# Optimization experiments

Measured on AMD Instinct MI355X. Metric: run time of the kernel, lower is better.

Reference implementation:

```python
import jax, jax.numpy as jnp
import numpy as np

# Problem dims (match init_kwargs)
M, P, TINI, NH, TT, NB = 4, 6, 50, 100, 2000, 4096
L = TT - TINI - NH + 1  # 1851, dimension of g
NC = TINI * M + TINI * P + P  # 506 equality constraints
DELTA = 1e-6  # tiny ridge on g so the KKT system is nonsingular (u,y unchanged to ~1e-6)


def block_hankel(w, Lr, d):
    """w: flat [T*d] time series (d-dim samples stacked). Returns [Lr*d, T-Lr+1].
    H[d*i+k, j] = w[d*(i+j)+k] = w[row + d*j]."""
    T = w.shape[0] // d
    cols = T - Lr + 1
    return w[jnp.arange(Lr * d)[:, None] + d * jnp.arange(cols)[None, :]]


def setup_inputs() -> dict:
    key = jax.random.key(0)
    ks = jax.random.split(key, 7)
    ud = jax.random.normal(ks[0], (TT, M), jnp.float32)          # input data series
    yd = jax.random.normal(ks[1], (TT, P), jnp.float32)          # output data series
    q = 10.0 + 0.1 * jax.random.normal(ks[2], (P * NH,), jnp.float32)  # diag of Q (positive)
    r = 10.0 + 0.1 * jax.random.normal(ks[3], (M * NH,), jnp.float32)  # diag of R (positive)
    ref = jax.random.normal(ks[4], (NB, NH * P), jnp.float32)
    u_ini = jax.random.normal(ks[5], (NB, TINI * M), jnp.float32)
    y_ini = jax.random.normal(ks[6], (NB, TINI * P), jnp.float32)
    return {"ud": ud, "yd": yd, "q": q, "r": r, "ref": ref, "u_ini": u_ini, "y_ini": y_ini}


def reference(ud, yd, q, r, ref, u_ini, y_ini):
    # Block-Hankel data matrices (the module's U, Y Parameters)
    U = block_hankel(ud.reshape(-1), TINI + NH, M)  # [(Tini+N)*m, L]
    Y = block_hankel(yd.reshape(-1), TINI + NH, P)  # [(Tini+N)*p, L]
    Up, Uf = U[: M * TINI], U[M * TINI:]            # [Tini*m, L], [N*m, L]
    Yp, Yf = Y[: P * TINI], Y[P * TINI:]            # [Tini*p, L], [N*p, L]

    # Deterministic (linear, non-stochastic) DeePC QP with inactive box constraints:
    #   min_g (Yf g - ref)^T Q (Yf g - ref) + (Uf g)^T R (Uf g)
    #   s.t.  Up g = u_ini, Yp g = y_ini, (Yf g)[-p:] = ref[-p:]
    # Solved exactly via the KKT system (unique in u = Uf g, y = Yf g).
    H = Yf.T @ (q[:, None] * Yf) + Uf.T @ (r[:, None] * Uf) + DELTA * jnp.eye(L, dtype=ud.dtype)
    A = jnp.concatenate([Up, Yp, Yf[-P:]], axis=0)  # [NC, L]
    KKT = jnp.block([
        [2.0 * H, A.T],
        [A, jnp.zeros((NC, NC), dtype=ud.dtype)],
    ])  # [L+NC, L+NC]

    rhs = jnp.concatenate([
        2.0 * (Yf.T @ (q[:, None] * ref.T)),  # [L, NB] gradient term
        u_ini.T,                               # [Tini*m, NB]
        y_ini.T,                               # [Tini*p, NB]
        ref[:, -P:].T,                          # [p, NB] terminal constraint
    ], axis=0)

    g = jnp.linalg.solve(KKT, rhs)[:L]  # [L, NB]
    inp = Uf @ g   # optimal input  [N*m, NB]
    out = Yf @ g   # optimal output [N*p, NB]
    return inp, out
```

## Files before the change

kernel.cpp:

```cpp
#include <hip/hip_runtime.h>
#include <hip/hip_bf16.h>

#define LDIM   1851
#define NFR    1000
#define NAR    506
#define NCRP   1536
#define LDC    1856
#define NG     1024
#define NS     512
#define NXC    1152
#define LDMA   1120
#define NBATCH 4096
#define NOUT   1000
#define INVDP  500000.0

#define OFF_C     ((size_t)0)
#define SZ_C      ((size_t)NCRP * LDC * 4)
#define OFF_ILG   OFF_C
#define OFF_ILS   (OFF_C + 8388608)
#define OFF_GCC   (OFF_C + SZ_C)
#define SZ_GCC    ((size_t)NCRP * NCRP * 8)
#define OFF_G     (OFF_GCC + SZ_GCC)
#define SZ_G      ((size_t)NG * NG * 8)
#define OFF_TA    (OFF_G + SZ_G)
#define SZ_TA     ((size_t)NG * NS * 8)
#define OFF_S     (OFF_TA + SZ_TA)
#define SZ_S      ((size_t)NS * NS * 8)
#define OFF_X12   (OFF_S + SZ_S)
#define SZ_X12    ((size_t)NS * NXC * 8)
#define OFF_MRAW  (OFF_X12 + SZ_X12)
#define SZ_MRAW   ((size_t)NG * NXC * 4)
#define OFF_XB    OFF_MRAW
#define OFF_MALL  (OFF_MRAW + SZ_MRAW)
#define SZ_MALL   ((size_t)NG * LDMA * 4)
#define OFF_IDG   OFF_MALL
#define OFF_IDS   (OFF_MALL + 524288)
#define OFF_INALL (OFF_MALL + SZ_MALL)
#define SZ_INALL  ((size_t)LDMA * NBATCH * 4)
#define OFF_TB    OFF_INALL
#define OFF_TINV  (OFF_INALL + 4194304)

__device__ __forceinline__ double dweight(int i, const float* q, const float* r) {
  return (i < 400) ? (double)r[i] : (double)q[i - 400];
}

__global__ __launch_bounds__(256) void k_build_C(const float* __restrict__ ud,
                                                 const float* __restrict__ yd,
                                                 float* __restrict__ C) {
  int j = blockIdx.x * 256 + threadIdx.x;
  int rr = blockIdx.y;
  if (j >= LDC) return;
  float v = 0.f;
  if (j < LDIM) {
    if (rr < 400)        v = ud[200 + rr + 4 * j];
    else if (rr < 1000)  v = yd[300 + (rr - 400) + 6 * j];
    else if (rr < 1200)  v = ud[(rr - 1000) + 4 * j];
    else if (rr < 1500)  v = yd[(rr - 1200) + 6 * j];
    else if (rr < 1506)  v = yd[894 + (rr - 1500) + 6 * j];
  }
  C[(size_t)rr * LDC + j] = v;
}

__global__ __launch_bounds__(256) void k_gram(const float* __restrict__ C,
                                              double* __restrict__ GCC) {
  int ti = blockIdx.y, tj = blockIdx.x;
  if (ti < tj) return;
  __shared__ float As[64][33];
  __shared__ float Bs[64][33];
  int tid = threadIdx.x;
  int tr4 = (tid >> 4) * 4, tc4 = (tid & 15) * 4;
  double acc[4][4] = {};
  int i0 = ti * 64, j0 = tj * 64;
  for (int k0 = 0; k0 < LDC; k0 += 32) {
#pragma unroll
    for (int l = 0; l < 8; ++l) {
      int t = tid + l * 256;
      int rr = t >> 5, cc = t & 31;
      As[rr][cc] = C[(size_t)(i0 + rr) * LDC + k0 + cc];
      Bs[rr][cc] = C[(size_t)(j0 + rr) * LDC + k0 + cc];
    }
    __syncthreads();
#pragma unroll
    for (int kk = 0; kk < 32; ++kk) {
      double a[4], b[4];
#pragma unroll
      for (int i = 0; i < 4; ++i) a[i] = (double)As[tr4 + i][kk];
#pragma unroll
      for (int jx = 0; jx < 4; ++jx) b[jx] = (double)Bs[tc4 + jx][kk];
#pragma unroll
      for (int i = 0; i < 4; ++i)
#pragma unroll
        for (int jx = 0; jx < 4; ++jx) acc[i][jx] += a[i] * b[jx];
    }
    __syncthreads();
  }
#pragma unroll
  for (int i = 0; i < 4; ++i)
#pragma unroll
    for (int jx = 0; jx < 4; ++jx) {
      int gi = i0 + tr4 + i, gj = j0 + tc4 + jx;
      GCC[(size_t)gi * NCRP + gj] = acc[i][jx];
      if (ti != tj) GCC[(size_t)gj * NCRP + gi] = acc[i][jx];
    }
}

__global__ __launch_bounds__(256) void k_copyG(const double* __restrict__ GCC,
                                               const float* __restrict__ q,
                                               const float* __restrict__ r,
                                               double* __restrict__ G) {
  int idx = blockIdx.x * 256 + threadIdx.x;
  int i = idx >> 10, j = idx & 1023;
  double v = (i < NFR && j < NFR) ? GCC[(size_t)i * NCRP + j] : 0.0;
  if (i == j) {
    if (i < NFR) v += 1e-6 / dweight(i, q, r);
    else v = 1.0;
  }
  G[idx] = v;
}

__global__ __launch_bounds__(256) void k_copyTA(const double* __restrict__ GCC,
                                                double* __restrict__ TA) {
  int idx = blockIdx.x * 256 + threadIdx.x;
  int f = idx >> 9, a = idx & 511;
  TA[idx] = (f < NFR && a < NAR) ? GCC[(size_t)f * NCRP + 1000 + a] : 0.0;
}

__global__ __launch_bounds__(256) void k_potrf_inv(double* __restrict__ M, int ld, int k,
                                                   double* __restrict__ IDG) {
  __shared__ double T[64][65];
  __shared__ double invd[64];
  int tid = threadIdx.x;
#pragma unroll
  for (int l = 0; l < 16; ++l) {
    int t = tid + l * 256;
    T[t >> 6][t & 63] = M[(size_t)(k + (t >> 6)) * ld + k + (t & 63)];
  }
  __syncthreads();
  for (int c = 0; c < 64; ++c) {
    if (tid == 0) T[c][c] = sqrt(T[c][c]);
    __syncthreads();
    double piv = T[c][c];
    for (int rr = c + 1 + tid; rr < 64; rr += 256) T[rr][c] /= piv;
    __syncthreads();
    for (int t = tid; t < 64 * 64; t += 256) {
      int rr = t >> 6, jj = t & 63;
      if (rr > c && jj > c) T[rr][jj] -= T[rr][c] * T[jj][c];
    }
    __syncthreads();
  }
#pragma unroll
  for (int l = 0; l < 16; ++l) {
    int t = tid + l * 256;
    M[(size_t)(k + (t >> 6)) * ld + k + (t & 63)] = T[t >> 6][t & 63];
  }
  __syncthreads();
  if (tid < 64) invd[tid] = 1.0 / T[tid][tid];
  __syncthreads();
  if (tid < 64) {
    int c = tid;
    for (int r = c + 1; r < 64; ++r) {
      double s = T[r][c] * invd[c];
      for (int j = c + 1; j < r; ++j) s += T[r][j] * T[c][j];
      T[c][r] = -s * invd[r];
    }
  }
  __syncthreads();
#pragma unroll
  for (int l = 0; l < 16; ++l) {
    int t = tid + l * 256;
    int r = t >> 6, c = t & 63;
    IDG[t] = (r < c) ? 0.0 : (r == c ? invd[r] : T[c][r]);
  }
}

__global__ __launch_bounds__(256) void k_trsm_inv(double* __restrict__ M, int ld, int k,
                                                  const double* __restrict__ IDG) {
  __shared__ double As[64][33];
  __shared__ double Bs[32][65];
  int tid = threadIdx.x;
  int tr4 = (tid >> 4) * 4, tc4 = (tid & 15) * 4;
  int r0 = k + 64 + blockIdx.x * 64;
  double acc[4][4] = {};
  for (int k0 = 0; k0 < 64; k0 += 32) {
#pragma unroll
    for (int l = 0; l < 8; ++l) {
      int t = tid + l * 256;
      As[t >> 5][t & 31] = M[(size_t)(r0 + (t >> 5)) * ld + k + k0 + (t & 31)];
    }
#pragma unroll
    for (int l = 0; l < 8; ++l) {
      int t = tid + l * 256;
      int kk = t >> 6, cc = t & 63;
      Bs[kk][cc] = IDG[cc * 64 + k0 + kk];
    }
    __syncthreads();
#pragma unroll
    for (int kk = 0; kk < 32; ++kk) {
      double a[4], b[4];
#pragma unroll
      for (int i = 0; i < 4; ++i) a[i] = As[tr4 + i][kk];
#pragma unroll
      for (int jx = 0; jx < 4; ++jx) b[jx] = Bs[kk][tc4 + jx];
#pragma unroll
      for (int i = 0; i < 4; ++i)
#pragma unroll
        for (int jx = 0; jx < 4; ++jx) acc[i][jx] += a[i] * b[jx];
    }
    __syncthreads();
  }
#pragma unroll
  for (int i = 0; i < 4; ++i)
#pragma unroll
    for (int jx = 0; jx < 4; ++jx)
      M[(size_t)(r0 + tr4 + i) * ld + k + tc4 + jx] = acc[i][jx];
}

__global__ __launch_bounds__(256) void k_chol_syrk(double* __restrict__ M, int ld, int k) {
  int ti = blockIdx.y, tj = blockIdx.x;
  if (ti < tj) return;
  __shared__ double Pa[64][33];
  __shared__ double Pb[64][33];
  int tid = threadIdx.x;
  int tr4 = (tid >> 4) * 4, tc4 = (tid & 15) * 4;
  int i0 = k + 64 + ti * 64, j0 = k + 64 + tj * 64;
  double acc[4][4] = {};
  for (int k0 = 0; k0 < 64; k0 += 32) {
#pragma unroll
    for (int l = 0; l < 8; ++l) {
      int t = tid + l * 256;
      int rr = t >> 5, cc = t & 31;
      Pa[rr][cc] = M[(size_t)(i0 + rr) * ld + k + k0 + cc];
      Pb[rr][cc] = M[(size_t)(j0 + rr) * ld + k + k0 + cc];
    }
    __syncthreads();
#pragma unroll
    for (int kk = 0; kk < 32; ++kk) {
      double a[4], b[4];
#pragma unroll
      for (int i = 0; i < 4; ++i) a[i] = Pa[tr4 + i][kk];
#pragma unroll
      for (int jx = 0; jx < 4; ++jx) b[jx] = Pb[tc4 + jx][kk];
#pragma unroll
      for (int i = 0; i < 4; ++i)
#pragma unroll
        for (int jx = 0; jx < 4; ++jx) acc[i][jx] += a[i] * b[jx];
    }
    __syncthreads();
  }
#pragma unroll
  for (int i = 0; i < 4; ++i)
#pragma unroll
    for (int jx = 0; jx < 4; ++jx)
      M[(size_t)(i0 + tr4 + i) * ld + j0 + tc4 + jx] -= acc[i][jx];
}

__device__ __forceinline__ void dgemm_nn_core(const double* __restrict__ A, int lda,
                                              const double* __restrict__ B, int ldb,
                                              double* __restrict__ C, int ldc,
                                              int kBeg, int kEnd, double alpha) {
  __shared__ double As[64][33];
  __shared__ double Bs[32][65];
  int tid = threadIdx.x;
  int tr4 = (tid >> 4) * 4, tc4 = (tid & 15) * 4;
  double acc[4][4] = {};
  for (int k0 = kBeg; k0 < kEnd; k0 += 32) {
#pragma unroll
    for (int l = 0; l < 8; ++l) {
      int t = tid + l * 256;
      As[t >> 5][t & 31] = A[(size_t)(t >> 5) * lda + k0 + (t & 31)];
    }
#pragma unroll
    for (int l = 0; l < 8; ++l) {
      int t = tid + l * 256;
      Bs[t >> 6][t & 63] = B[(size_t)(k0 + (t >> 6)) * ldb + (t & 63)];
    }
    __syncthreads();
#pragma unroll
    for (int kk = 0; kk < 32; ++kk) {
      double a[4], b[4];
#pragma unroll
      for (int i = 0; i < 4; ++i) a[i] = As[tr4 + i][kk];
#pragma unroll
      for (int jx = 0; jx < 4; ++jx) b[jx] = Bs[kk][tc4 + jx];
#pragma unroll
      for (int i = 0; i < 4; ++i)
#pragma unroll
        for (int jx = 0; jx < 4; ++jx) acc[i][jx] += a[i] * b[jx];
    }
    __syncthreads();
  }
#pragma unroll
  for (int i = 0; i < 4; ++i)
#pragma unroll
    for (int jx = 0; jx < 4; ++jx)
      C[(size_t)(tr4 + i) * ldc + tc4 + jx] = alpha * acc[i][jx];
}

__device__ __forceinline__ void dgemm_tn_core(const double* __restrict__ A, int lda,
                                              const double* __restrict__ B, int ldb,
                                              double* __restrict__ C, int ldc,
                                              int kBeg, int kEnd, double alpha) {
  __shared__ double Ls[32][65];
  __shared__ double Bs[32][65];
  int tid = threadIdx.x;
  int tr4 = (tid >> 4) * 4, tc4 = (tid & 15) * 4;
  double acc[4][4] = {};
  for (int k0 = kBeg; k0 < kEnd; k0 += 32) {
#pragma unroll
    for (int l = 0; l < 8; ++l) {
      int t = tid + l * 256;
      int jj = t >> 6, rr = t & 63;
      Ls[jj][rr] = A[(size_t)(k0 + jj) * lda + rr];
    }
#pragma unroll
    for (int l = 0; l < 8; ++l) {
      int t = tid + l * 256;
      Bs[t >> 6][t & 63] = B[(size_t)(k0 + (t >> 6)) * ldb + (t & 63)];
    }
    __syncthreads();
#pragma unroll
    for (int kk = 0; kk < 32; ++kk) {
      double a[4], b[4];
#pragma unroll
      for (int i = 0; i < 4; ++i) a[i] = Ls[kk][tr4 + i];
#pragma unroll
      for (int jx = 0; jx < 4; ++jx) b[jx] = Bs[kk][tc4 + jx];
#pragma unroll
      for (int i = 0; i < 4; ++i)
#pragma unroll
        for (int jx = 0; jx < 4; ++jx) acc[i][jx] += a[i] * b[jx];
    }
    __syncthreads();
  }
#pragma unroll
  for (int i = 0; i < 4; ++i)
#pragma unroll
    for (int jx = 0; jx < 4; ++jx)
      C[(size_t)(tr4 + i) * ldc + tc4 + jx] = alpha * acc[i][jx];
}

__global__ __launch_bounds__(256) void k_dgemm_nn(const double* __restrict__ A, int lda,
                                                  const double* __restrict__ B, int ldb,
                                                  double* __restrict__ C, int ldc,
                                                  int K, int tri, double alpha) {
  int bi = blockIdx.y, bj = blockIdx.x;
  int kEnd = tri ? ((bi + 1) * 64 < K ? (bi + 1) * 64 : K) : K;
  dgemm_nn_core(A + (size_t)bi * 64 * lda, lda, B + bj * 64, ldb,
                C + (size_t)bi * 64 * ldc + bj * 64, ldc, 0, kEnd, alpha);
}

__global__ __launch_bounds__(256) void k_dgemm_tn(const double* __restrict__ A, int lda,
                                                  const double* __restrict__ B, int ldb,
                                                  double* __restrict__ C, int ldc,
                                                  int K, int tri, double alpha) {
  int bi = blockIdx.y, bj = blockIdx.x;
  int kBeg = tri ? bi * 64 : 0;
  dgemm_tn_core(A + bi * 64, lda, B + bj * 64, ldb,
                C + (size_t)bi * 64 * ldc + bj * 64, ldc, kBeg, K, alpha);
}

__global__ __launch_bounds__(256) void k_init_iL(double* __restrict__ iL, int nShift,
                                                 const double* __restrict__ IDIAG) {
  int idx = blockIdx.x * 256 + threadIdx.x;
  int n = 1 << nShift;
  int i = idx >> nShift, j = idx & (n - 1);
  int d = i >> 6;
  double v = 0.0;
  if ((j >> 6) == d) v = IDIAG[(size_t)d * 4096 + (i & 63) * 64 + (j & 63)];
  iL[idx] = v;
}

__global__ __launch_bounds__(256) void k_ilv_tmp(const double* __restrict__ L, int ldl,
                                                 const double* __restrict__ iL, int ldi,
                                                 double* __restrict__ T, int half) {
  int p = blockIdx.z, bi = blockIdx.y, bj = blockIdx.x;
  int base = p * 2 * half;
  dgemm_nn_core(L + (size_t)(base + half + bi * 64) * ldl + base, ldl,
                iL + (size_t)base * ldi + base + bj * 64, ldi,
                T + (size_t)p * half * half + (size_t)bi * 64 * half + bj * 64, half,
                0, half, 1.0);
}

__global__ __launch_bounds__(256) void k_ilv_fin(double* __restrict__ iL, int ldi,
                                                 const double* __restrict__ T, int half) {
  int p = blockIdx.z, bi = blockIdx.y, bj = blockIdx.x;
  int base = p * 2 * half;
  dgemm_nn_core(iL + (size_t)(base + half + bi * 64) * ldi + base + half, ldi,
                T + (size_t)p * half * half + bj * 64, half,
                iL + (size_t)(base + half + bi * 64) * ldi + base + bj * 64, ldi,
                0, half, -1.0);
}

__global__ __launch_bounds__(256) void k_buildS(const double* __restrict__ GCC,
                                                const double* __restrict__ TA,
                                                double* __restrict__ S) {
  __shared__ double Ga[64][33];
  __shared__ double Tb[32][65];
  int tid = threadIdx.x;
  int tr4 = (tid >> 4) * 4, tc4 = (tid & 15) * 4;
  int a0 = blockIdx.y * 64, b0 = blockIdx.x * 64;
  double acc[4][4] = {};
  for (int f0 = 0; f0 < NG; f0 += 32) {
#pragma unroll
    for (int l = 0; l < 8; ++l) {
      int t = tid + l * 256;
      int rr = t >> 5, cc = t & 31;
      Ga[rr][cc] = GCC[(size_t)(1000 + a0 + rr) * NCRP + f0 + cc];
    }
#pragma unroll
    for (int l = 0; l < 8; ++l) {
      int t = tid + l * 256;
      int rr = t >> 6, cc = t & 63;
      Tb[rr][cc] = TA[(size_t)(f0 + rr) * NS + b0 + cc];
    }
    __syncthreads();
#pragma unroll
    for (int kk = 0; kk < 32; ++kk) {
      double a[4], b[4];
#pragma unroll
      for (int i = 0; i < 4; ++i) a[i] = Ga[tr4 + i][kk];
#pragma unroll
      for (int jx = 0; jx < 4; ++jx) b[jx] = Tb[kk][tc4 + jx];
#pragma unroll
      for (int i = 0; i < 4; ++i)
#pragma unroll
        for (int jx = 0; jx < 4; ++jx) acc[i][jx] += a[i] * b[jx];
    }
    __syncthreads();
  }
#pragma unroll
  for (int i = 0; i < 4; ++i)
#pragma unroll
    for (int jx = 0; jx < 4; ++jx) {
      int a = a0 + tr4 + i, b = b0 + tc4 + jx;
      double v;
      if (a < NAR && b < NAR)
        v = (GCC[(size_t)(1000 + a) * NCRP + 1000 + b] - acc[i][jx]) * INVDP;
      else
        v = (a == b) ? 1.0 : 0.0;
      S[(size_t)a * NS + b] = v;
    }
}

__global__ __launch_bounds__(256) void k_build_x12rhs(const double* __restrict__ TA,
                                                      double* __restrict__ X12) {
  int c = blockIdx.x * 256 + threadIdx.x;
  int a = blockIdx.y;
  if (c >= NXC) return;
  double v = 0.0;
  if (a < NAR) {
    if (c < 600) v = TA[(size_t)(400 + c) * NS + a];
    else if (c < 1106) v = (a == (c - 600)) ? 1.0 : 0.0;
  }
  X12[(size_t)a * NXC + c] = v;
}

__global__ __launch_bounds__(256) void k_gemm_M(const double* __restrict__ TA,
                                                const double* __restrict__ X12,
                                                const float* __restrict__ q,
                                                const float* __restrict__ r,
                                                float* __restrict__ Mraw) {
  __shared__ double Ga[64][33];
  __shared__ double Xb[32][65];
  int tid = threadIdx.x;
  int tr4 = (tid >> 4) * 4, tc4 = (tid & 15) * 4;
  int o0 = blockIdx.y * 64, c0 = blockIdx.x * 64;
  double acc[4][4] = {};
  for (int k0 = 0; k0 < NS; k0 += 32) {
#pragma unroll
    for (int l = 0; l < 8; ++l) {
      int t = tid + l * 256;
      int rr = t >> 5, cc = t & 31;
      Ga[rr][cc] = TA[(size_t)(o0 + rr) * NS + k0 + cc];
    }
#pragma unroll
    for (int l = 0; l < 8; ++l) {
      int t = tid + l * 256;
      int rr = t >> 6, cc = t & 63;
      Xb[rr][cc] = X12[(size_t)(k0 + rr) * NXC + c0 + cc];
    }
    __syncthreads();
#pragma unroll
    for (int kk = 0; kk < 32; ++kk) {
      double a[4], b[4];
#pragma unroll
      for (int i = 0; i < 4; ++i) a[i] = Ga[tr4 + i][kk];
#pragma unroll
      for (int jx = 0; jx < 4; ++jx) b[jx] = Xb[kk][tc4 + jx];
#pragma unroll
      for (int i = 0; i < 4; ++i)
#pragma unroll
        for (int jx = 0; jx < 4; ++jx) acc[i][jx] += a[i] * b[jx];
    }
    __syncthreads();
  }
#pragma unroll
  for (int i = 0; i < 4; ++i)
#pragma unroll
    for (int jx = 0; jx < 4; ++jx) {
      int o = o0 + tr4 + i, col = c0 + tc4 + jx;
      float v = 0.f;
      if (o < NFR) {
        double scale = 1.0 / (2.0 * dweight(o, q, r));
        double t = acc[i][jx] * scale;
        v = (float)((col < 600) ? -t : t);
      }
      Mraw[(size_t)o * NXC + col] = v;
    }
}

__global__ __launch_bounds__(256) void k_assemble_M(const float* __restrict__ Mraw,
                                                    float* __restrict__ Mall) {
  int j = blockIdx.x * 256 + threadIdx.x;
  int o = blockIdx.y;
  if (j >= LDMA) return;
  float v = 0.f;
  if (j < 600) {
    v = Mraw[(size_t)o * NXC + j];
    if (o == 400 + j) v += 1.0f;
    if (j >= 594) v += Mraw[(size_t)o * NXC + 1100 + (j - 594)];
  } else if (j < 1100) {
    v = Mraw[(size_t)o * NXC + j];
  }
  Mall[(size_t)o * LDMA + j] = v;
}

__global__ __launch_bounds__(256) void k_transpose_in(const float* __restrict__ ref,
                                                      const float* __restrict__ ui,
                                                      const float* __restrict__ yi,
                                                      float* __restrict__ INall) {
  __shared__ float t[32][33];
  int tx = threadIdx.x & 31, ty = threadIdx.x >> 5;
  int n0 = blockIdx.x * 32, j0 = blockIdx.y * 32;
#pragma unroll
  for (int p = 0; p < 4; ++p) {
    int nb = n0 + ty + p * 8;
    int j = j0 + tx;
    float v = 0.f;
    if (j < 600)        v = ref[(size_t)nb * 600 + j];
    else if (j < 800)   v = ui[(size_t)nb * 200 + (j - 600)];
    else if (j < 1100)  v = yi[(size_t)nb * 300 + (j - 800)];
    t[ty + p * 8][tx] = v;
  }
  __syncthreads();
#pragma unroll
  for (int p = 0; p < 4; ++p) {
    INall[(size_t)(j0 + ty + p * 8) * NBATCH + n0 + tx] = t[tx][ty + p * 8];
  }
}

__global__ __launch_bounds__(256) void k_gemm_out(const float* __restrict__ Mall,
                                                  const float* __restrict__ INall,
                                                  float* __restrict__ out) {
  __shared__ float As[32][132];
  __shared__ float Bs[32][132];
  int tid = threadIdx.x;
  int tr = tid >> 4, tc = tid & 15;
  int m0 = blockIdx.y * 128, n0 = blockIdx.x * 128;
  float acc[8][8] = {};
  for (int k0 = 0; k0 < LDMA; k0 += 32) {
#pragma unroll
    for (int l = 0; l < 16; ++l) {
      int t = tid + l * 256;
      int rr = t >> 5, cc = t & 31;
      As[cc][rr] = Mall[(size_t)(m0 + rr) * LDMA + k0 + cc];
    }
#pragma unroll
    for (int l = 0; l < 16; ++l) {
      int t = tid + l * 256;
      int rr = t >> 7, cc = t & 127;
      Bs[rr][cc] = INall[(size_t)(k0 + rr) * NBATCH + n0 + cc];
    }
    __syncthreads();
#pragma unroll
    for (int kk = 0; kk < 32; ++kk) {
      float4 a0 = *(const float4*)&As[kk][tr * 4];
      float4 a1 = *(const float4*)&As[kk][64 + tr * 4];
      float4 b0 = *(const float4*)&Bs[kk][tc * 4];
      float4 b1 = *(const float4*)&Bs[kk][64 + tc * 4];
      float av[8] = {a0.x, a0.y, a0.z, a0.w, a1.x, a1.y, a1.z, a1.w};
      float bv[8] = {b0.x, b0.y, b0.z, b0.w, b1.x, b1.y, b1.z, b1.w};
#pragma unroll
      for (int i = 0; i < 8; ++i)
#pragma unroll
        for (int jx = 0; jx < 8; ++jx) acc[i][jx] += av[i] * bv[jx];
    }
    __syncthreads();
  }
#pragma unroll
  for (int ih = 0; ih < 2; ++ih)
#pragma unroll
    for (int i = 0; i < 4; ++i) {
      int o = m0 + ih * 64 + tr * 4 + i;
      if (o < NOUT) {
#pragma unroll
        for (int jh = 0; jh < 2; ++jh) {
          float4 v = make_float4(acc[ih * 4 + i][jh * 4 + 0], acc[ih * 4 + i][jh * 4 + 1],
                                 acc[ih * 4 + i][jh * 4 + 2], acc[ih * 4 + i][jh * 4 + 3]);
          *(float4*)&out[(size_t)o * NBATCH + n0 + jh * 64 + tc * 4] = v;
        }
      }
    }
}

extern "C" void kernel_launch(void* const* d_in, const int* in_sizes, int n_in,
                              void* d_out, int out_size, void* d_ws, size_t ws_size,
                              hipStream_t stream) {
  const float* ud  = (const float*)d_in[0];
  const float* yd  = (const float*)d_in[1];
  const float* qv  = (const float*)d_in[2];
  const float* rv  = (const float*)d_in[3];
  const float* ref = (const float*)d_in[4];
  const float* ui  = (const float*)d_in[5];
  const float* yi  = (const float*)d_in[6];
  float* out = (float*)d_out;
  char* w = (char*)d_ws;

  float*  C    = (float*)(w + OFF_C);
  double* GCC  = (double*)(w + OFF_GCC);
  double* G    = (double*)(w + OFF_G);
  double* TA   = (double*)(w + OFF_TA);
  double* S    = (double*)(w + OFF_S);
  double* X12  = (double*)(w + OFF_X12);
  float*  MRAW = (float*)(w + OFF_MRAW);
  float*  MALL = (float*)(w + OFF_MALL);
  float*  INA  = (float*)(w + OFF_INALL);
  double* ILG  = (double*)(w + OFF_ILG);
  double* ILS  = (double*)(w + OFF_ILS);
  double* IDG  = (double*)(w + OFF_IDG);
  double* IDS  = (double*)(w + OFF_IDS);
  double* TB   = (double*)(w + OFF_TB);
  double* TINV = (double*)(w + OFF_TINV);
  double* XB   = (double*)(w + OFF_XB);

  k_build_C<<<dim3(8, NCRP), 256, 0, stream>>>(ud, yd, C);
  k_gram<<<dim3(24, 24), 256, 0, stream>>>(C, GCC);
  k_copyG<<<dim3(NG * NG / 256), 256, 0, stream>>>(GCC, qv, rv, G);
  k_copyTA<<<dim3(NG * NS / 256), 256, 0, stream>>>(GCC, TA);

  for (int k = 0; k < NG; k += 64) {
    k_potrf_inv<<<1, 256, 0, stream>>>(G, NG, k, IDG + (size_t)(k >> 6) * 4096);
    int nb = (NG - k - 64) / 64;
    if (nb > 0) {
      k_trsm_inv<<<dim3(nb), 256, 0, stream>>>(G, NG, k, IDG + (size_t)(k >> 6) * 4096);
      k_chol_syrk<<<dim3(nb, nb), 256, 0, stream>>>(G, NG, k);
    }
  }

  k_init_iL<<<dim3(NG * NG / 256), 256, 0, stream>>>(ILG, 10, IDG);
  for (int lv = 0; lv < 4; ++lv) {
    int half = 64 << lv, pairs = NG / (2 * half);
    dim3 gt(half / 64, half / 64, pairs);
    k_ilv_tmp<<<gt, 256, 0, stream>>>(G, NG, ILG, NG, TINV, half);
    k_ilv_fin<<<gt, 256, 0, stream>>>(ILG, NG, TINV, half);
  }
  k_dgemm_nn<<<dim3(NS / 64, NG / 64), 256, 0, stream>>>(ILG, NG, TA, NS, TB, NS, NG, 1, 1.0);
  k_dgemm_tn<<<dim3(NS / 64, NG / 64), 256, 0, stream>>>(ILG, NG, TB, NS, TA, NS, NG, 1, 1.0);

  k_buildS<<<dim3(8, 8), 256, 0, stream>>>(GCC, TA, S);
  for (int k = 0; k < NS; k += 64) {
    k_potrf_inv<<<1, 256, 0, stream>>>(S, NS, k, IDS + (size_t)(k >> 6) * 4096);
    int nb = (NS - k - 64) / 64;
    if (nb > 0) {
      k_trsm_inv<<<dim3(nb), 256, 0, stream>>>(S, NS, k, IDS + (size_t)(k >> 6) * 4096);
      k_chol_syrk<<<dim3(nb, nb), 256, 0, stream>>>(S, NS, k);
    }
  }
  k_init_iL<<<dim3(NS * NS / 256), 256, 0, stream>>>(ILS, 9, IDS);
  for (int lv = 0; lv < 3; ++lv) {
    int half = 64 << lv, pairs = NS / (2 * half);
    dim3 gt(half / 64, half / 64, pairs);
    k_ilv_tmp<<<gt, 256, 0, stream>>>(S, NS, ILS, NS, TINV, half);
    k_ilv_fin<<<gt, 256, 0, stream>>>(ILS, NS, TINV, half);
  }

  k_build_x12rhs<<<dim3(5, NS), 256, 0, stream>>>(TA, X12);
  k_dgemm_nn<<<dim3(NXC / 64, NS / 64), 256, 0, stream>>>(ILS, NS, X12, NXC, XB, NXC, NS, 1, 1.0);
  k_dgemm_tn<<<dim3(NXC / 64, NS / 64), 256, 0, stream>>>(ILS, NS, XB, NXC, X12, NXC, NS, 1, 1.0);

  k_gemm_M<<<dim3(NXC / 64, NG / 64), 256, 0, stream>>>(TA, X12, qv, rv, MRAW);
  k_assemble_M<<<dim3(5, NG), 256, 0, stream>>>(MRAW, MALL);
  k_transpose_in<<<dim3(NBATCH / 32, LDMA / 32), 256, 0, stream>>>(ref, ui, yi, INA);
  k_gemm_out<<<dim3(NBATCH / 128, NG / 128), 256, 0, stream>>>(MALL, INA, out);
}
```

Baseline: 5.104 ms.

## Fuse blocked Cholesky panel, trsm and syrk into one kernel per step

```diff
diff --git a/kernel.cpp b/kernel.cpp
--- a/kernel.cpp
+++ b/kernel.cpp
@@ -35,10 +35,14 @@
 #define SZ_MALL   ((size_t)NG * LDMA * 4)
 #define OFF_IDG   OFF_MALL
 #define OFF_IDS   (OFF_MALL + 524288)
+#define OFF_WG    (OFF_MALL + 786432)
+#define OFF_WS    (OFF_MALL + 1310720)
+#define OFF_LS    (OFF_MALL + 1572864)
 #define OFF_INALL (OFF_MALL + SZ_MALL)
 #define SZ_INALL  ((size_t)LDMA * NBATCH * 4)
 #define OFF_TB    OFF_INALL
 #define OFF_TINV  (OFF_INALL + 4194304)
+#define OFF_LG    (OFF_INALL + 6291456)
 
 __device__ __forceinline__ double dweight(int i, const float* q, const float* r) {
   return (i < 400) ? (double)r[i] : (double)q[i - 400];
@@ -63,44 +67,48 @@
 
 __global__ __launch_bounds__(256) void k_gram(const float* __restrict__ C,
                                               double* __restrict__ GCC) {
-  int ti = blockIdx.y, tj = blockIdx.x;
-  if (ti < tj) return;
-  __shared__ float As[64][33];
+  int ti = blockIdx.y;
+  int tj = blockIdx.x;
+  if (ti * 32 + 31 < tj * 64) return;
+  __shared__ float As[32][33];
   __shared__ float Bs[64][33];
   int tid = threadIdx.x;
-  int tr4 = (tid >> 4) * 4, tc4 = (tid & 15) * 4;
-  double acc[4][4] = {};
-  int i0 = ti * 64, j0 = tj * 64;
+  int tr2 = (tid >> 4) * 2, tc4 = (tid & 15) * 4;
+  double acc[2][4] = {};
+  int i0 = ti * 32, j0 = tj * 64;
   for (int k0 = 0; k0 < LDC; k0 += 32) {
 #pragma unroll
-    for (int l = 0; l < 8; ++l) {
-      int t = tid + l * 256;
-      int rr = t >> 5, cc = t & 31;
-      As[rr][cc] = C[(size_t)(i0 + rr) * LDC + k0 + cc];
-      Bs[rr][cc] = C[(size_t)(j0 + rr) * LDC + k0 + cc];
+    for (int l = 0; l < 4; ++l) {
+      int t = tid + l * 256;
+      As[t >> 5][t & 31] = C[(size_t)(i0 + (t >> 5)) * LDC + k0 + (t & 31)];
+    }
+#pragma unroll
+    for (int l = 0; l < 8; ++l) {
+      int t = tid + l * 256;
+      Bs[t >> 5][t & 31] = C[(size_t)(j0 + (t >> 5)) * LDC + k0 + (t & 31)];
     }
     __syncthreads();
 #pragma unroll
     for (int kk = 0; kk < 32; ++kk) {
-      double a[4], b[4];
-#pragma unroll
-      for (int i = 0; i < 4; ++i) a[i] = (double)As[tr4 + i][kk];
+      double a[2], b[4];
+#pragma unroll
+      for (int i = 0; i < 2; ++i) a[i] = (double)As[tr2 + i][kk];
 #pragma unroll
       for (int jx = 0; jx < 4; ++jx) b[jx] = (double)Bs[tc4 + jx][kk];
 #pragma unroll
-      for (int i = 0; i < 4; ++i)
+      for (int i = 0; i < 2; ++i)
 #pragma unroll
         for (int jx = 0; jx < 4; ++jx) acc[i][jx] += a[i] * b[jx];
     }
     __syncthreads();
   }
 #pragma unroll
-  for (int i = 0; i < 4; ++i)
+  for (int i = 0; i < 2; ++i)
 #pragma unroll
     for (int jx = 0; jx < 4; ++jx) {
-      int gi = i0 + tr4 + i, gj = j0 + tc4 + jx;
+      int gi = i0 + tr2 + i, gj = j0 + tc4 + jx;
       GCC[(size_t)gi * NCRP + gj] = acc[i][jx];
-      if (ti != tj) GCC[(size_t)gj * NCRP + gi] = acc[i][jx];
+      if (gi > gj) GCC[(size_t)gj * NCRP + gi] = acc[i][jx];
     }
 }
 
@@ -125,43 +133,36 @@
   TA[idx] = (f < NFR && a < NAR) ? GCC[(size_t)f * NCRP + 1000 + a] : 0.0;
 }
 
-__global__ __launch_bounds__(256) void k_potrf_inv(double* __restrict__ M, int ld, int k,
-                                                   double* __restrict__ IDG) {
-  __shared__ double T[64][65];
-  __shared__ double invd[64];
-  int tid = threadIdx.x;
+__device__ __forceinline__ void potrf_inv_w(double* sm, int tid,
+                                            double* Ldst, int ld,
+                                            double* iLout, double* Wout) {
+  double* invd = sm + 4160;
+  for (int c = 0; c < 64; ++c) {
+    if (tid == 0) sm[c * 65 + c] = sqrt(sm[c * 65 + c]);
+    __syncthreads();
+    double piv = sm[c * 65 + c];
+    for (int rr = c + 1 + tid; rr < 64; rr += 256) sm[rr * 65 + c] /= piv;
+    __syncthreads();
+    for (int t = tid; t < 64 * 64; t += 256) {
+      int rr = t >> 6, jj = t & 63;
+      if (rr > c && jj > c) sm[rr * 65 + jj] -= sm[rr * 65 + c] * sm[jj * 65 + c];
+    }
+    __syncthreads();
+  }
 #pragma unroll
   for (int l = 0; l < 16; ++l) {
     int t = tid + l * 256;
-    T[t >> 6][t & 63] = M[(size_t)(k + (t >> 6)) * ld + k + (t & 63)];
+    Ldst[(size_t)(t >> 6) * ld + (t & 63)] = sm[(t >> 6) * 65 + (t & 63)];
   }
   __syncthreads();
-  for (int c = 0; c < 64; ++c) {
-    if (tid == 0) T[c][c] = sqrt(T[c][c]);
-    __syncthreads();
-    double piv = T[c][c];
-    for (int rr = c + 1 + tid; rr < 64; rr += 256) T[rr][c] /= piv;
-    __syncthreads();
-    for (int t = tid; t < 64 * 64; t += 256) {
-      int rr = t >> 6, jj = t & 63;
-      if (rr > c && jj > c) T[rr][jj] -= T[rr][c] * T[jj][c];
-    }
-    __syncthreads();
-  }
-#pragma unroll
-  for (int l = 0; l < 16; ++l) {
-    int t = tid + l * 256;
-    M[(size_t)(k + (t >> 6)) * ld + k + (t & 63)] = T[t >> 6][t & 63];
-  }
-  __syncthreads();
-  if (tid < 64) invd[tid] = 1.0 / T[tid][tid];
+  if (tid < 64) invd[tid] = 1.0 / sm[tid * 65 + tid];
   __syncthreads();
   if (tid < 64) {
     int c = tid;
     for (int r = c + 1; r < 64; ++r) {
-      double s = T[r][c] * invd[c];
-      for (int j = c + 1; j < r; ++j) s += T[r][j] * T[c][j];
-      T[c][r] = -s * invd[r];
+      double s = sm[r * 65 + c] * invd[c];
+      for (int j = c + 1; j < r; ++j) s += sm[r * 65 + j] * sm[c * 65 + j];
+      sm[c * 65 + r] = -s * invd[r];
     }
   }
   __syncthreads();
@@ -169,89 +170,159 @@
   for (int l = 0; l < 16; ++l) {
     int t = tid + l * 256;
     int r = t >> 6, c = t & 63;
-    IDG[t] = (r < c) ? 0.0 : (r == c ? invd[r] : T[c][r]);
-  }
-}
-
-__global__ __launch_bounds__(256) void k_trsm_inv(double* __restrict__ M, int ld, int k,
-                                                  const double* __restrict__ IDG) {
-  __shared__ double As[64][33];
-  __shared__ double Bs[32][65];
+    iLout[t] = (r < c) ? 0.0 : (r == c ? invd[r] : sm[c * 65 + r]);
+  }
+  for (int idx = tid; idx < 4096; idx += 256) {
+    int r = idx >> 6, c = idx & 63;
+    int k2 = r > c ? r : c;
+    double s = 0.0;
+    for (; k2 < 64; ++k2) {
+      double ar = (k2 == r) ? invd[r] : sm[r * 65 + k2];
+      double ac = (k2 == c) ? invd[c] : sm[c * 65 + k2];
+      s += ar * ac;
+    }
+    Wout[idx] = s;
+  }
+}
+
+__global__ __launch_bounds__(256) void k_potrf_inv0(double* __restrict__ M, int ld,
+                                                    double* __restrict__ LG,
+                                                    double* __restrict__ iL0,
+                                                    double* __restrict__ W0) {
+  __shared__ double sm[4160 + 64];
   int tid = threadIdx.x;
+#pragma unroll
+  for (int l = 0; l < 16; ++l) {
+    int t = tid + l * 256;
+    sm[(t >> 6) * 65 + (t & 63)] = M[(size_t)(t >> 6) * ld + (t & 63)];
+  }
+  __syncthreads();
+  potrf_inv_w(sm, tid, LG, ld, iL0, W0);
+}
+
+#define FS1(r, c) sm[(r) * 65 + (c)]
+#define FS2(r, c) sm[4160 + (r) * 33 + (c)]
+__global__ __launch_bounds__(256) void k_chol_fused(double* __restrict__ M, int ld, int k,
+                                                    const double* __restrict__ iLcur,
+                                                    const double* __restrict__ Wcur,
+                                                    double* __restrict__ LG,
+                                                    double* __restrict__ iLnext,
+                                                    double* __restrict__ Wnext) {
+  __shared__ double sm[6272];
+  int tid = threadIdx.x;
+  int t = blockIdx.x;
+  int i = (int)((sqrtf(8.f * t + 1.f) - 1.f) * 0.5f);
+  while ((i + 1) * (i + 2) / 2 <= t) ++i;
+  while (i * (i + 1) / 2 > t) --i;
+  int j = t - i * (i + 1) / 2;
   int tr4 = (tid >> 4) * 4, tc4 = (tid & 15) * 4;
-  int r0 = k + 64 + blockIdx.x * 64;
+  int rowAi = k + 64 + i * 64, rowAj = k + 64 + j * 64;
+
+  if (j == 0) {
+#pragma unroll
+    for (int l = 0; l < 16; ++l) { int t2 = tid + l * 256; FS1(t2 >> 6, t2 & 63) = iLcur[t2]; }
+    __syncthreads();
+    double li[4][4] = {};
+    for (int k0 = 0; k0 < 64; k0 += 32) {
+#pragma unroll
+      for (int l = 0; l < 8; ++l) {
+        int t2 = tid + l * 256;
+        FS2(t2 >> 5, t2 & 31) = M[(size_t)(rowAi + (t2 >> 5)) * ld + k + k0 + (t2 & 31)];
+      }
+      __syncthreads();
+#pragma unroll
+      for (int mm = 0; mm < 32; ++mm) {
+        double a[4], b[4];
+#pragma unroll
+        for (int i2 = 0; i2 < 4; ++i2) a[i2] = FS2(tr4 + i2, mm);
+#pragma unroll
+        for (int j2 = 0; j2 < 4; ++j2) b[j2] = FS1(tc4 + j2, k0 + mm);
+#pragma unroll
+        for (int i2 = 0; i2 < 4; ++i2)
+#pragma unroll
+          for (int j2 = 0; j2 < 4; ++j2) li[i2][j2] += a[i2] * b[j2];
+      }
+      __syncthreads();
+    }
+#pragma unroll
+    for (int i2 = 0; i2 < 4; ++i2)
+#pragma unroll
+      for (int j2 = 0; j2 < 4; ++j2)
+        LG[(size_t)(rowAi + tr4 + i2) * ld + k + tc4 + j2] = li[i2][j2];
+  }
+  __syncthreads();
+
+#pragma unroll
+  for (int l = 0; l < 16; ++l) { int t2 = tid + l * 256; FS1(t2 >> 6, t2 & 63) = Wcur[t2]; }
+  __syncthreads();
   double acc[4][4] = {};
   for (int k0 = 0; k0 < 64; k0 += 32) {
 #pragma unroll
     for (int l = 0; l < 8; ++l) {
-      int t = tid + l * 256;
-      As[t >> 5][t & 31] = M[(size_t)(r0 + (t >> 5)) * ld + k + k0 + (t & 31)];
-    }
-#pragma unroll
-    for (int l = 0; l < 8; ++l) {
-      int t = tid + l * 256;
-      int kk = t >> 6, cc = t & 63;
-      Bs[kk][cc] = IDG[cc * 64 + k0 + kk];
-    }
-    __syncthreads();
-#pragma unroll
-    for (int kk = 0; kk < 32; ++kk) {
+      int t2 = tid + l * 256;
+      FS2(t2 >> 5, t2 & 31) = M[(size_t)(rowAj + (t2 >> 5)) * ld + k + k0 + (t2 & 31)];
+    }
+    __syncthreads();
+#pragma unroll
+    for (int mm = 0; mm < 32; ++mm) {
       double a[4], b[4];
 #pragma unroll
-      for (int i = 0; i < 4; ++i) a[i] = As[tr4 + i][kk];
-#pragma unroll
-      for (int jx = 0; jx < 4; ++jx) b[jx] = Bs[kk][tc4 + jx];
-#pragma unroll
-      for (int i = 0; i < 4; ++i)
-#pragma unroll
-        for (int jx = 0; jx < 4; ++jx) acc[i][jx] += a[i] * b[jx];
-    }
-    __syncthreads();
-  }
-#pragma unroll
-  for (int i = 0; i < 4; ++i)
-#pragma unroll
-    for (int jx = 0; jx < 4; ++jx)
-      M[(size_t)(r0 + tr4 + i) * ld + k + tc4 + jx] = acc[i][jx];
-}
-
-__global__ __launch_bounds__(256) void k_chol_syrk(double* __restrict__ M, int ld, int k) {
-  int ti = blockIdx.y, tj = blockIdx.x;
-  if (ti < tj) return;
-  __shared__ double Pa[64][33];
-  __shared__ double Pb[64][33];
-  int tid = threadIdx.x;
-  int tr4 = (tid >> 4) * 4, tc4 = (tid & 15) * 4;
-  int i0 = k + 64 + ti * 64, j0 = k + 64 + tj * 64;
-  double acc[4][4] = {};
+      for (int i2 = 0; i2 < 4; ++i2) a[i2] = FS1(tr4 + i2, k0 + mm);
+#pragma unroll
+      for (int j2 = 0; j2 < 4; ++j2) b[j2] = FS2(tc4 + j2, mm);
+#pragma unroll
+      for (int i2 = 0; i2 < 4; ++i2)
+#pragma unroll
+        for (int j2 = 0; j2 < 4; ++j2) acc[i2][j2] += a[i2] * b[j2];
+    }
+    __syncthreads();
+  }
+#pragma unroll
+  for (int i2 = 0; i2 < 4; ++i2)
+#pragma unroll
+    for (int j2 = 0; j2 < 4; ++j2) FS1(tr4 + i2, tc4 + j2) = acc[i2][j2];
+  __syncthreads();
+  double acc2[4][4] = {};
   for (int k0 = 0; k0 < 64; k0 += 32) {
 #pragma unroll
     for (int l = 0; l < 8; ++l) {
-      int t = tid + l * 256;
-      int rr = t >> 5, cc = t & 31;
-      Pa[rr][cc] = M[(size_t)(i0 + rr) * ld + k + k0 + cc];
-      Pb[rr][cc] = M[(size_t)(j0 + rr) * ld + k + k0 + cc];
-    }
-    __syncthreads();
-#pragma unroll
-    for (int kk = 0; kk < 32; ++kk) {
+      int t2 = tid + l * 256;
+      FS2(t2 >> 5, t2 & 31) = M[(size_t)(rowAi + (t2 >> 5)) * ld + k + k0 + (t2 & 31)];
+    }
+    __syncthreads();
+#pragma unroll
+    for (int mm = 0; mm < 32; ++mm) {
       double a[4], b[4];
 #pragma unroll
-      for (int i = 0; i < 4; ++i) a[i] = Pa[tr4 + i][kk];
-#pragma unroll
-      for (int jx = 0; jx < 4; ++jx) b[jx] = Pb[tc4 + jx][kk];
-#pragma unroll
-      for (int i = 0; i < 4; ++i)
-#pragma unroll
-        for (int jx = 0; jx < 4; ++jx) acc[i][jx] += a[i] * b[jx];
-    }
-    __syncthreads();
-  }
-#pragma unroll
-  for (int i = 0; i < 4; ++i)
-#pragma unroll
-    for (int jx = 0; jx < 4; ++jx)
-      M[(size_t)(i0 + tr4 + i) * ld + j0 + tc4 + jx] -= acc[i][jx];
+      for (int i2 = 0; i2 < 4; ++i2) a[i2] = FS2(tr4 + i2, mm);
+#pragma unroll
+      for (int j2 = 0; j2 < 4; ++j2) b[j2] = FS1(k0 + mm, tc4 + j2);
+#pragma unroll
+      for (int i2 = 0; i2 < 4; ++i2)
+#pragma unroll
+        for (int j2 = 0; j2 < 4; ++j2) acc2[i2][j2] += a[i2] * b[j2];
+    }
+    __syncthreads();
+  }
+  double upd[4][4];
+#pragma unroll
+  for (int i2 = 0; i2 < 4; ++i2)
+#pragma unroll
+    for (int j2 = 0; j2 < 4; ++j2) {
+      size_t off = (size_t)(rowAi + tr4 + i2) * ld + rowAj + tc4 + j2;
+      upd[i2][j2] = M[off] - acc2[i2][j2];
+      M[off] = upd[i2][j2];
+    }
+
+  if (blockIdx.x == 0) {
+    __syncthreads();
+#pragma unroll
+    for (int i2 = 0; i2 < 4; ++i2)
+#pragma unroll
+      for (int j2 = 0; j2 < 4; ++j2) FS1(tr4 + i2, tc4 + j2) = upd[i2][j2];
+    __syncthreads();
+    potrf_inv_w(sm, tid, LG + (size_t)(k + 64) * ld + (k + 64), ld, iLnext, Wnext);
+  }
 }
 
 __device__ __forceinline__ void dgemm_nn_core(const double* __restrict__ A, int lda,
@@ -404,14 +475,12 @@
 #pragma unroll
     for (int l = 0; l < 8; ++l) {
       int t = tid + l * 256;
-      int rr = t >> 5, cc = t & 31;
-      Ga[rr][cc] = GCC[(size_t)(1000 + a0 + rr) * NCRP + f0 + cc];
-    }
-#pragma unroll
-    for (int l = 0; l < 8; ++l) {
-      int t = tid + l * 256;
-      int rr = t >> 6, cc = t & 63;
-      Tb[rr][cc] = TA[(size_t)(f0 + rr) * NS + b0 + cc];
+      Ga[t >> 5][t & 31] = GCC[(size_t)(1000 + a0 + (t >> 5)) * NCRP + f0 + (t & 31)];
+    }
+#pragma unroll
+    for (int l = 0; l < 8; ++l) {
+      int t = tid + l * 256;
+      Tb[t >> 6][t & 63] = TA[(size_t)(f0 + (t >> 6)) * NS + b0 + (t & 63)];
     }
     __syncthreads();
 #pragma unroll
@@ -470,14 +539,12 @@
 #pragma unroll
     for (int l = 0; l < 8; ++l) {
       int t = tid + l * 256;
-      int rr = t >> 5, cc = t & 31;
-      Ga[rr][cc] = TA[(size_t)(o0 + rr) * NS + k0 + cc];
-    }
-#pragma unroll
-    for (int l = 0; l < 8; ++l) {
-      int t = tid + l * 256;
-      int rr = t >> 6, cc = t & 63;
-      Xb[rr][cc] = X12[(size_t)(k0 + rr) * NXC + c0 + cc];
+      Ga[t >> 5][t & 31] = TA[(size_t)(o0 + (t >> 5)) * NS + k0 + (t & 31)];
+    }
+#pragma unroll
+    for (int l = 0; l < 8; ++l) {
+      int t = tid + l * 256;
+      Xb[t >> 6][t & 63] = X12[(size_t)(k0 + (t >> 6)) * NXC + c0 + (t & 63)];
     }
     __syncthreads();
 #pragma unroll
@@ -502,8 +569,8 @@
       float v = 0.f;
       if (o < NFR) {
         double scale = 1.0 / (2.0 * dweight(o, q, r));
-        double t = acc[i][jx] * scale;
-        v = (float)((col < 600) ? -t : t);
+        double tt = acc[i][jx] * scale;
+        v = (float)((col < 600) ? -tt : tt);
       }
       Mraw[(size_t)o * NXC + col] = v;
     }
@@ -629,48 +696,50 @@
   double* ILS  = (double*)(w + OFF_ILS);
   double* IDG  = (double*)(w + OFF_IDG);
   double* IDS  = (double*)(w + OFF_IDS);
+  double* WG   = (double*)(w + OFF_WG);
+  double* WS   = (double*)(w + OFF_WS);
+  double* LG   = (double*)(w + OFF_LG);
+  double* LS   = (double*)(w + OFF_LS);
   double* TB   = (double*)(w + OFF_TB);
   double* TINV = (double*)(w + OFF_TINV);
   double* XB   = (double*)(w + OFF_XB);
 
   k_build_C<<<dim3(8, NCRP), 256, 0, stream>>>(ud, yd, C);
-  k_gram<<<dim3(24, 24), 256, 0, stream>>>(C, GCC);
+  k_gram<<<dim3(24, 48), 256, 0, stream>>>(C, GCC);
   k_copyG<<<dim3(NG * NG / 256), 256, 0, stream>>>(GCC, qv, rv, G);
   k_copyTA<<<dim3(NG * NS / 256), 256, 0, stream>>>(GCC, TA);
 
-  for (int k = 0; k < NG; k += 64) {
-    k_potrf_inv<<<1, 256, 0, stream>>>(G, NG, k, IDG + (size_t)(k >> 6) * 4096);
-    int nb = (NG - k - 64) / 64;
-    if (nb > 0) {
-      k_trsm_inv<<<dim3(nb), 256, 0, stream>>>(G, NG, k, IDG + (size_t)(k >> 6) * 4096);
-      k_chol_syrk<<<dim3(nb, nb), 256, 0, stream>>>(G, NG, k);
-    }
+  k_potrf_inv0<<<1, 256, 0, stream>>>(G, NG, LG, IDG, WG);
+  for (int p = 0; p < 15; ++p) {
+    int nb = 15 - p;
+    k_chol_fused<<<dim3(nb * (nb + 1) / 2), 256, 0, stream>>>(
+        G, NG, p * 64, IDG + (size_t)p * 4096, WG + (size_t)p * 4096, LG,
+        IDG + (size_t)(p + 1) * 4096, WG + (size_t)(p + 1) * 4096);
   }
 
   k_init_iL<<<dim3(NG * NG / 256), 256, 0, stream>>>(ILG, 10, IDG);
   for (int lv = 0; lv < 4; ++lv) {
     int half = 64 << lv, pairs = NG / (2 * half);
     dim3 gt(half / 64, half / 64, pairs);
-    k_ilv_tmp<<<gt, 256, 0, stream>>>(G, NG, ILG, NG, TINV, half);
+    k_ilv_tmp<<<gt, 256, 0, stream>>>(LG, NG, ILG, NG, TINV, half);
     k_ilv_fin<<<gt, 256, 0, stream>>>(ILG, NG, TINV, half);
   }
   k_dgemm_nn<<<dim3(NS / 64, NG / 64), 256, 0, stream>>>(ILG, NG, TA, NS, TB, NS, NG, 1, 1.0);
   k_dgemm_tn<<<dim3(NS / 64, NG / 64), 256, 0, stream>>>(ILG, NG, TB, NS, TA, NS, NG, 1, 1.0);
 
   k_buildS<<<dim3(8, 8), 256, 0, stream>>>(GCC, TA, S);
-  for (int k = 0; k < NS; k += 64) {
-    k_potrf_inv<<<1, 256, 0, stream>>>(S, NS, k, IDS + (size_t)(k >> 6) * 4096);
-    int nb = (NS - k - 64) / 64;
-    if (nb > 0) {
-      k_trsm_inv<<<dim3(nb), 256, 0, stream>>>(S, NS, k, IDS + (size_t)(k >> 6) * 4096);
-      k_chol_syrk<<<dim3(nb, nb), 256, 0, stream>>>(S, NS, k);
-    }
+  k_potrf_inv0<<<1, 256, 0, stream>>>(S, NS, LS, IDS, WS);
+  for (int p = 0; p < 7; ++p) {
+    int nb = 7 - p;
+    k_chol_fused<<<dim3(nb * (nb + 1) / 2), 256, 0, stream>>>(
+        S, NS, p * 64, IDS + (size_t)p * 4096, WS + (size_t)p * 4096, LS,
+        IDS + (size_t)(p + 1) * 4096, WS + (size_t)(p + 1) * 4096);
   }
   k_init_iL<<<dim3(NS * NS / 256), 256, 0, stream>>>(ILS, 9, IDS);
   for (int lv = 0; lv < 3; ++lv) {
     int half = 64 << lv, pairs = NS / (2 * half);
     dim3 gt(half / 64, half / 64, pairs);
-    k_ilv_tmp<<<gt, 256, 0, stream>>>(S, NS, ILS, NS, TINV, half);
+    k_ilv_tmp<<<gt, 256, 0, stream>>>(LS, NS, ILS, NS, TINV, half);
     k_ilv_fin<<<gt, 256, 0, stream>>>(ILS, NS, TINV, half);
   }
 
```

Measured after the change: 5.889 ms. 1.15x slower.
